# Optimization experiments

Hardware: AMD Instinct MI355X
Metric: run time of the kernel (lower is better)

The kernel has to match this reference:

```python
import jax, jax.numpy as jnp
import numpy as np

B, S, R, H = 32, 512, 49, 768


def setup_inputs() -> dict:
    key = jax.random.key(0)
    ks = jax.random.split(key, 32)
    rn = lambda i, shape, s=1.0: jax.random.normal(ks[i], shape, dtype=jnp.float32) * s
    W = 0.05  # weight init scale to keep tanh/softmax in a sane range
    return {
        'text_features': rn(0, (B, S, H)),
        'img_features': rn(1, (B, R, H)),
        't1_w': rn(2, (H, H), W), 't1_b': rn(3, (H,), W),
        'i1_w': rn(4, (H, H), W),
        'a1_w': rn(5, (2 * H,), W), 'a1_b': rn(6, (), W),
        't2_w': rn(7, (H, H), W),
        'i2_w': rn(8, (H, H), W), 'i2_b': rn(9, (H,), W),
        'a2_w': rn(10, (2 * H,), W), 'a2_b': rn(11, (), W),
        'gt_w': rn(12, (H, H), W), 'gt_b': rn(13, (H,), W),
        'gi_w': rn(14, (H, H), W), 'gi_b': rn(15, (H,), W),
        'gg_w': rn(16, (2 * H, 1), W), 'gg_b': rn(17, (1,), W),
        'ft_w': rn(18, (H, H), W),
        'fm_w': rn(19, (H, H), W), 'fm_b': rn(20, (H,), W),
        'fg_w': rn(21, (2 * H, 1), W), 'fg_b': rn(22, (1,), W),
        'fr_w': rn(23, (H, H), W), 'fr_b': rn(24, (H,), W),
    }


def reference(text_features, img_features, t1_w, t1_b, i1_w, a1_w, a1_b,
              t2_w, i2_w, i2_b, a2_w, a2_b, gt_w, gt_b, gi_w, gi_b,
              gg_w, gg_b, ft_w, fm_w, fm_b, fg_w, fg_b, fr_w, fr_b):
    H = text_features.shape[-1]
    # --- CoAttention, stage 1 (text attends over image regions) ---
    # tanh(concat) is elementwise and att_linear_1 is rank-1, so split the score:
    # score[b,s,r] = tanh(t1(x_s)) . a1[:H] + tanh(i1(y_r)) . a1[H:] + b
    t_sc = jnp.tanh(text_features @ t1_w + t1_b) @ a1_w[:H]          # (B,S)
    i_sc = jnp.tanh(img_features @ i1_w) @ a1_w[H:]                  # (B,R)
    visual_att = jax.nn.softmax(t_sc[:, :, None] + i_sc[:, None, :] + a1_b, axis=-1)  # (B,S,R)
    att_img = jnp.einsum('bsr,brh->bsh', visual_att, img_features)   # (B,S,H)
    # --- CoAttention, stage 2 (attended-image queries attend over text) ---
    # concat order is [img, text] -> a2[:H] pairs with img part
    q_sc = jnp.tanh(att_img @ i2_w + i2_b) @ a2_w[:H]                # (B,S)
    k_sc = jnp.tanh(text_features @ t2_w) @ a2_w[H:]                 # (B,S)
    textual_att = jax.nn.softmax(q_sc[:, :, None] + k_sc[:, None, :] + a2_b, axis=-1)  # (B,S,S)
    att_text = jnp.einsum('bij,bjh->bih', textual_att, text_features)  # (B,S,H)
    # --- GMF gated fusion ---
    new_img = jnp.tanh(att_img @ gi_w + gi_b)
    new_txt = jnp.tanh(att_text @ gt_w + gt_b)
    gate = jax.nn.sigmoid(jnp.concatenate([new_img, new_txt], axis=-1) @ gg_w + gg_b)  # (B,S,1)
    multimodal = gate * new_img + (1.0 - gate) * new_txt
    # --- filtration gate ---
    concat_feat = jnp.concatenate([text_features @ ft_w, multimodal @ fm_w + fm_b], axis=-1)
    fgate = jax.nn.sigmoid(concat_feat @ fg_w + fg_b)                # (B,S,1)
    return fgate * jnp.tanh(multimodal @ fr_w + fr_b)
```

## Files before the change

### kernel.cpp

```cpp
#include <hip/hip_runtime.h>
#include <hip/hip_bf16.h>
#include <math.h>

constexpr int BD = 32;
constexpr int SD = 512;
constexpr int RD = 49;
constexpr int HD = 768;
constexpr int MT = BD * SD;
constexpr int MI = BD * RD;
constexpr int NP = 12;
constexpr int MBT = MT / 128;
constexpr int MBI = 13;
constexpr int NWG = (MBT + MBI) * 6;
constexpr int NT2 = HD / 64;

typedef __bf16 bf16;
typedef __bf16 bf16x4 __attribute__((ext_vector_type(4)));
typedef __bf16 bf16x8 __attribute__((ext_vector_type(8)));
typedef float f32x4 __attribute__((ext_vector_type(4)));

#define GLOAD_LDS16(g, l) __builtin_amdgcn_global_load_lds( \
    (__attribute__((address_space(1))) void*)(g),           \
    (__attribute__((address_space(3))) void*)(l), 16, 0, 0)

__device__ __forceinline__ float fast_tanh(float x) {
    const float e = __expf(2.f * x);
    return 1.f - 2.f / (e + 1.f);
}

__global__ __launch_bounds__(256) void prep_text(
    const float* __restrict__ text, const float* __restrict__ v_f,
    bf16* __restrict__ text_bf, float* __restrict__ s_txt)
{
    const int row = blockIdx.x * 4 + (threadIdx.x >> 6);
    const int lane = threadIdx.x & 63;
    const float* tr = text + (size_t)row * HD;
    bf16* tb = text_bf + (size_t)row * HD;
    float acc = 0.f;
    #pragma unroll
    for (int c = 0; c < 3; ++c) {
        const int o = c * 256 + lane * 4;
        const f32x4 x = *(const f32x4*)(tr + o);
        const f32x4 v = *(const f32x4*)(v_f + o);
        bf16x4 b; b[0] = (bf16)x[0]; b[1] = (bf16)x[1]; b[2] = (bf16)x[2]; b[3] = (bf16)x[3];
        *(bf16x4*)(tb + o) = b;
        acc += x[0] * v[0] + x[1] * v[1] + x[2] * v[2] + x[3] * v[3];
    }
    for (int off = 32; off; off >>= 1) acc += __shfl_xor(acc, off);
    if (lane == 0) s_txt[row] = acc;
}

__global__ __launch_bounds__(256) void prep_misc(
    const float* __restrict__ ft_w, const float* __restrict__ fm_w,
    const float* __restrict__ fm_b, const float* __restrict__ fg_w,
    float* __restrict__ v_f, float* __restrict__ v_m, float* __restrict__ c_m,
    const float* __restrict__ img, bf16* __restrict__ img_bf,
    const float* __restrict__ t2_w, const float* __restrict__ i1_w,
    bf16* __restrict__ wt_t, bf16* __restrict__ wt_i)
{
    __shared__ float tile[64][65];
    const int bid = blockIdx.x;
    if (bid < 385) {
        const int idx = bid * 4 + (threadIdx.x >> 6);
        const int lane = threadIdx.x & 63;
        const float* row; const float* vecp; float* outp;
        if (idx < HD)            { row = ft_w + (size_t)idx * HD;        vecp = fg_w;      outp = v_f + idx; }
        else if (idx < 2 * HD)   { row = fm_w + (size_t)(idx - HD) * HD; vecp = fg_w + HD; outp = v_m + (idx - HD); }
        else if (idx == 2 * HD)  { row = fm_b;                           vecp = fg_w + HD; outp = c_m; }
        else return;
        float acc = 0.f;
        #pragma unroll
        for (int i = 0; i < HD / 64; ++i) acc += row[lane + 64 * i] * vecp[lane + 64 * i];
        for (int off = 32; off; off >>= 1) acc += __shfl_xor(acc, off);
        if (lane == 0) *outp = acc;
    } else if (bid < 385 + 588) {
        const int i = (bid - 385) * 256 + threadIdx.x;
        const int n8 = BD * RD * HD / 8;
        if (i >= n8) return;
        const size_t o = (size_t)i * 8;
        const f32x4 x0 = *(const f32x4*)(img + o);
        const f32x4 x1 = *(const f32x4*)(img + o + 4);
        bf16x8 b;
        b[0]=(bf16)x0[0]; b[1]=(bf16)x0[1]; b[2]=(bf16)x0[2]; b[3]=(bf16)x0[3];
        b[4]=(bf16)x1[0]; b[5]=(bf16)x1[1]; b[6]=(bf16)x1[2]; b[7]=(bf16)x1[3];
        *(bf16x8*)(img_bf + o) = b;
    } else {
        const int idx2 = bid - (385 + 588);
        const int z = idx2 / 144, rem = idx2 % 144;
        const int bx = rem % 12, by = rem / 12;
        const float* W = z ? i1_w : t2_w;
        bf16* Wt = z ? wt_i : wt_t;
        const int k0 = bx * 64, n0 = by * 64;
        const int t = threadIdx.x;
        const int rb = t >> 6, c = t & 63;
        #pragma unroll
        for (int i = 0; i < 16; ++i) {
            const int r = rb + i * 4;
            tile[r][c] = W[(size_t)(k0 + r) * HD + n0 + c];
        }
        __syncthreads();
        #pragma unroll
        for (int i = 0; i < 16; ++i) {
            const int r = rb + i * 4;
            Wt[(size_t)(n0 + r) * HD + k0 + c] = (bf16)tile[c][r];
        }
    }
}

__global__ __launch_bounds__(256, 4) void gemm2(
    const bf16* __restrict__ Atext, const bf16* __restrict__ WtT,
    const float* __restrict__ vecT, float* __restrict__ partT,
    const bf16* __restrict__ Aimg, const bf16* __restrict__ WtI,
    const float* __restrict__ vecI, float* __restrict__ partI)
{
    __shared__ __align__(16) bf16 As[16 * 512];
    __shared__ __align__(16) bf16 Bs[16 * 512];

    const int bid = blockIdx.x;
    const int q = NWG / 8, r = NWG % 8;
    const int xcd = bid % 8, sidx = bid / 8;
    const int o = (xcd < r ? xcd * (q + 1) : r * (q + 1) + (xcd - r) * q) + sidx;
    const int mb = o / 6, nb = o % 6;

    const bool isT = mb < MBT;
    const bf16* A    = isT ? Atext : Aimg;
    const bf16* Wt   = isT ? WtT : WtI;
    const float* vec = isT ? vecT : vecI;
    float* part      = isT ? partT : partI;
    const int m0 = (isT ? mb : mb - MBT) * 128;
    const int n0 = nb * 128;

    const int t = threadIdx.x;
    const int w = t >> 6, lane = t & 63;
    const int quad = lane >> 4, l16 = lane & 15;
    const int wm2 = (w >> 1) * 64, wn2 = (w & 1) * 64;

    const bf16* Ag = A  + (size_t)(m0 + l16) * HD + quad * 8;
    const bf16* Bg = Wt + (size_t)(n0 + l16) * HD + quad * 8;

    f32x4 acc[4][4] = {};

    for (int tt = 0; tt < NT2; ++tt) {
        const int kk = tt * 64;
        #pragma unroll
        for (int h = 0; h < 2; ++h) {
            #pragma unroll
            for (int j = 0; j < 2; ++j) {
                const int rc = 2 * w + j;
                GLOAD_LDS16(Ag + (size_t)rc * 16 * HD + kk + h * 32, As + (h * 8 + rc) * 512);
                GLOAD_LDS16(Bg + (size_t)rc * 16 * HD + kk + h * 32, Bs + (h * 8 + rc) * 512);
            }
        }
        __syncthreads();

        #pragma unroll
        for (int h = 0; h < 2; ++h) {
            bf16x8 af[4], bg4[4];
            #pragma unroll
            for (int f = 0; f < 4; ++f) {
                af[f]  = *(const bf16x8*)(As + (h * 8 + wm2 / 16 + f) * 512 + lane * 8);
                bg4[f] = *(const bf16x8*)(Bs + (h * 8 + wn2 / 16 + f) * 512 + lane * 8);
            }
            #pragma unroll
            for (int fi = 0; fi < 4; ++fi)
                #pragma unroll
                for (int fj = 0; fj < 4; ++fj)
                    acc[fi][fj] = __builtin_amdgcn_mfma_f32_16x16x32_bf16(af[fi], bg4[fj], acc[fi][fj], 0, 0, 0);
        }
        __syncthreads();
    }

    float vv[4];
    #pragma unroll
    for (int fj = 0; fj < 4; ++fj) vv[fj] = vec[n0 + wn2 + fj * 16 + l16];

    #pragma unroll
    for (int fi = 0; fi < 4; ++fi) {
        #pragma unroll
        for (int reg = 0; reg < 4; ++reg) {
            float p = 0.f;
            #pragma unroll
            for (int fj = 0; fj < 4; ++fj)
                p += fast_tanh(acc[fi][fj][reg]) * vv[fj];
            p += __shfl_xor(p, 1);
            p += __shfl_xor(p, 2);
            p += __shfl_xor(p, 4);
            p += __shfl_xor(p, 8);
            if (l16 == 0) {
                const int row = m0 + wm2 + fi * 16 + quad * 4 + reg;
                part[(size_t)row * NP + nb * 2 + (w & 1)] = p;
            }
        }
    }
}

__global__ __launch_bounds__(256) void red_soft(
    const float* __restrict__ k_part, const float* __restrict__ i_part,
    float* __restrict__ k_sc, float* __restrict__ i_sc)
{
    __shared__ float red[4];
    if (blockIdx.x < BD) {
        const int b = blockIdx.x, t = threadIdx.x;
        const float* p0 = k_part + ((size_t)b * SD + t) * NP;
        const float* p1 = k_part + ((size_t)b * SD + 256 + t) * NP;
        float x0 = 0.f, x1 = 0.f;
        #pragma unroll
        for (int j = 0; j < 3; ++j) {
            const f32x4 a = *(const f32x4*)(p0 + j * 4);
            const f32x4 c = *(const f32x4*)(p1 + j * 4);
            x0 += a[0] + a[1] + a[2] + a[3];
            x1 += c[0] + c[1] + c[2] + c[3];
        }
        float m = fmaxf(x0, x1);
        for (int off = 32; off; off >>= 1) m = fmaxf(m, __shfl_xor(m, off));
        if ((t & 63) == 0) red[t >> 6] = m;
        __syncthreads();
        m = fmaxf(fmaxf(red[0], red[1]), fmaxf(red[2], red[3]));
        const float e0 = expf(x0 - m), e1 = expf(x1 - m);
        float s = e0 + e1;
        for (int off = 32; off; off >>= 1) s += __shfl_xor(s, off);
        __syncthreads();
        if ((t & 63) == 0) red[t >> 6] = s;
        __syncthreads();
        s = red[0] + red[1] + red[2] + red[3];
        k_sc[b * SD + t] = e0 / s;
        k_sc[b * SD + 256 + t] = e1 / s;
    } else {
        const int b = blockIdx.x - BD, l = threadIdx.x;
        if (l < 64) {
            float x = -1e30f;
            if (l < RD) {
                const float* p = i_part + ((size_t)(b * RD + l)) * NP;
                float s0 = 0.f;
                #pragma unroll
                for (int j = 0; j < 3; ++j) {
                    const f32x4 a = *(const f32x4*)(p + j * 4);
                    s0 += a[0] + a[1] + a[2] + a[3];
                }
                x = s0;
            }
            float m = x;
            for (int off = 32; off; off >>= 1) m = fmaxf(m, __shfl_xor(m, off));
            float e = (l < RD) ? expf(x - m) : 0.f;
            float s = e;
            for (int off = 32; off; off >>= 1) s += __shfl_xor(s, off);
            if (l < RD) i_sc[b * RD + l] = e / s;
        }
    }
}

__global__ __launch_bounds__(256) void wsum_both(
    const float* __restrict__ P1, const float* __restrict__ img,
    float* __restrict__ aimg,
    const float* __restrict__ P2, const bf16* __restrict__ text_bf,
    float* __restrict__ ws_part)
{
    __shared__ float Ps[SD];
    const int bid = blockIdx.x;
    if (bid < 96) {
        const int b = bid & 31, hy = bid >> 5;
        const int h = hy * 256 + threadIdx.x;
        for (int j = threadIdx.x; j < RD; j += 256) Ps[j] = P1[b * RD + j];
        __syncthreads();
        float acc = 0.f;
        const float* Xb = img + (size_t)b * RD * HD + h;
        for (int j = 0; j < RD; ++j) acc += Ps[j] * Xb[(size_t)j * HD];
        aimg[b * HD + h] = acc;
    } else {
        const int idx = bid - 96;
        const int q = idx / 96, rem = idx % 96;
        const int b = rem & 31, hy = rem >> 5;
        const int h = hy * 256 + threadIdx.x;
        if (threadIdx.x < 128) Ps[threadIdx.x] = P2[b * SD + q * 128 + threadIdx.x];
        __syncthreads();
        float acc = 0.f;
        const bf16* Xb = text_bf + (size_t)b * SD * HD + (size_t)(q * 128) * HD + h;
        #pragma unroll 8
        for (int j = 0; j < 128; ++j) acc += Ps[j] * (float)Xb[(size_t)j * HD];
        ws_part[((size_t)(b * 4 + q)) * HD + h] = acc;
    }
}

__global__ __launch_bounds__(256) void ni_nt_kernel(
    const float* __restrict__ aimg, const float* __restrict__ ws_part,
    const float* __restrict__ gi_w, const float* __restrict__ gi_b,
    const float* __restrict__ gt_w, const float* __restrict__ gt_b,
    float* __restrict__ ni, float* __restrict__ nt)
{
    const int b = blockIdx.x, n0 = blockIdx.y * 64, which = blockIdx.z;
    const float* W = which ? gt_w : gi_w;
    const float* bias = which ? gt_b : gi_b;
    float* Y = which ? nt : ni;

    __shared__ float Xs[HD];
    __shared__ float partial[4][64];
    const int t = threadIdx.x;
    if (which) {
        for (int h = t; h < HD; h += 256)
            Xs[h] = ws_part[((size_t)(b * 4 + 0)) * HD + h] + ws_part[((size_t)(b * 4 + 1)) * HD + h]
                  + ws_part[((size_t)(b * 4 + 2)) * HD + h] + ws_part[((size_t)(b * 4 + 3)) * HD + h];
    } else {
        for (int h = t; h < HD; h += 256) Xs[h] = aimg[b * HD + h];
    }
    __syncthreads();
    const int n = n0 + (t & 63), kq = t >> 6;
    float acc = 0.f;
    const float* Wp = W + (size_t)(kq * 192) * HD + n;
    #pragma unroll 8
    for (int h = 0; h < 192; ++h) acc += Xs[kq * 192 + h] * Wp[(size_t)h * HD];
    partial[kq][t & 63] = acc;
    __syncthreads();
    if (t < 64) {
        const float s = partial[0][t] + partial[1][t] + partial[2][t] + partial[3][t];
        Y[b * HD + n0 + t] = tanhf(s + bias[n0 + t]);
    }
}

__global__ __launch_bounds__(256) void gateT(
    const float* __restrict__ ni, const float* __restrict__ nt,
    const float* __restrict__ gg_w, const float* __restrict__ gg_b,
    const float* __restrict__ v_m, const float* __restrict__ c_m,
    const float* __restrict__ fg_b,
    const float* __restrict__ fr_w, const float* __restrict__ fr_b,
    float* __restrict__ T, float* __restrict__ s_mm)
{
    const int b = blockIdx.x, n0 = blockIdx.y * 64, t = threadIdx.x;
    __shared__ float Ni[HD], Nt[HD], Mm[HD];
    __shared__ float partial[4][64];
    __shared__ float red[4];
    __shared__ float gsh;

    float acc = 0.f;
    for (int n = t; n < HD; n += 256) {
        const float vi = ni[b * HD + n], vt = nt[b * HD + n];
        Ni[n] = vi; Nt[n] = vt;
        acc += vi * gg_w[n] + vt * gg_w[HD + n];
    }
    for (int off = 32; off; off >>= 1) acc += __shfl_xor(acc, off);
    if ((t & 63) == 0) red[t >> 6] = acc;
    __syncthreads();
    if (t == 0) gsh = 1.f / (1.f + expf(-(red[0] + red[1] + red[2] + red[3] + gg_b[0])));
    __syncthreads();
    const float g = gsh;
    float a2 = 0.f;
    for (int n = t; n < HD; n += 256) {
        const float m = g * Ni[n] + (1.f - g) * Nt[n];
        Mm[n] = m;
        a2 += m * v_m[n];
    }
    __syncthreads();
    const int n = n0 + (t & 63), kq = t >> 6;
    float tacc = 0.f;
    const float* Wp = fr_w + (size_t)(kq * 192) * HD + n;
    #pragma unroll 8
    for (int h = 0; h < 192; ++h) tacc += Mm[kq * 192 + h] * Wp[(size_t)h * HD];
    partial[kq][t & 63] = tacc;
    if (blockIdx.y == 0) {
        for (int off = 32; off; off >>= 1) a2 += __shfl_xor(a2, off);
        __syncthreads();
        if ((t & 63) == 0) red[t >> 6] = a2;
        __syncthreads();
        if (t == 0) s_mm[b] = red[0] + red[1] + red[2] + red[3] + *c_m + fg_b[0];
    } else {
        __syncthreads();
    }
    __syncthreads();
    if (t < 64) {
        const float s = partial[0][t] + partial[1][t] + partial[2][t] + partial[3][t];
        T[b * HD + n0 + t] = tanhf(s + fr_b[n0 + t]);
    }
}

__global__ __launch_bounds__(256) void out_kernel(const float* __restrict__ s_txt,
                                                  const float* __restrict__ s_mm,
                                                  const float* __restrict__ T,
                                                  float* __restrict__ out) {
    const size_t idx = ((size_t)blockIdx.x * 256 + threadIdx.x) * 4;
    const int h = (int)(idx % HD);
    const int bs = (int)(idx / HD);
    const int b = bs >> 9;
    float f = s_txt[bs] + s_mm[b];
    f = 1.f / (1.f + expf(-f));
    const float* Tp = T + b * HD + h;
    f32x4 o;
    o[0] = f * Tp[0]; o[1] = f * Tp[1]; o[2] = f * Tp[2]; o[3] = f * Tp[3];
    *(f32x4*)(out + idx) = o;
}

extern "C" void kernel_launch(void* const* d_in, const int* in_sizes, int n_in,
                              void* d_out, int out_size, void* d_ws, size_t ws_size,
                              hipStream_t stream) {
    const float* text = (const float*)d_in[0];
    const float* img  = (const float*)d_in[1];
    const float* i1_w = (const float*)d_in[4];
    const float* a1_w = (const float*)d_in[5];
    const float* t2_w = (const float*)d_in[7];
    const float* a2_w = (const float*)d_in[10];
    const float* gt_w = (const float*)d_in[12];
    const float* gt_b = (const float*)d_in[13];
    const float* gi_w = (const float*)d_in[14];
    const float* gi_b = (const float*)d_in[15];
    const float* gg_w = (const float*)d_in[16];
    const float* gg_b = (const float*)d_in[17];
    const float* ft_w = (const float*)d_in[18];
    const float* fm_w = (const float*)d_in[19];
    const float* fm_b = (const float*)d_in[20];
    const float* fg_w = (const float*)d_in[21];
    const float* fg_b = (const float*)d_in[22];
    const float* fr_w = (const float*)d_in[23];
    const float* fr_b = (const float*)d_in[24];
    float* out = (float*)d_out;

    float* sc_ = out;
    float* i_part  = sc_;
    float* k_part  = sc_ + 38400;
    float* i_sc    = sc_ + 431616;
    float* k_sc    = sc_ + 433216;
    float* aimg    = sc_ + 449600;
    float* v_f     = sc_ + 498752;
    float* v_m     = sc_ + 499520;
    float* c_m     = sc_ + 500288;
    float* ws_part = sc_ + 500352;
    float* ni      = sc_ + 598656;
    float* nt      = sc_ + 623232;
    bf16* text_bf  = (bf16*)(sc_ + 672384);
    bf16* img_bf   = (bf16*)(sc_ + 6963840);
    bf16* wt_t     = (bf16*)(sc_ + 7565952);
    bf16* wt_i     = (bf16*)(sc_ + 7860864);

    float* ws    = (float*)d_ws;
    float* s_txt = ws;
    float* s_mm  = ws + 16384;
    float* T     = ws + 16448;

    prep_misc<<<dim3(385 + 588 + 288), dim3(256), 0, stream>>>(
        ft_w, fm_w, fm_b, fg_w, v_f, v_m, c_m, img, img_bf, t2_w, i1_w, wt_t, wt_i);
    prep_text<<<dim3(MT / 4), dim3(256), 0, stream>>>(text, v_f, text_bf, s_txt);
    gemm2<<<dim3(NWG), dim3(256), 0, stream>>>(
        text_bf, wt_t, a2_w + HD, k_part, img_bf, wt_i, a1_w + HD, i_part);
    red_soft<<<dim3(2 * BD), dim3(256), 0, stream>>>(k_part, i_part, k_sc, i_sc);
    wsum_both<<<dim3(96 + 384), dim3(256), 0, stream>>>(
        i_sc, img, aimg, k_sc, text_bf, ws_part);
    ni_nt_kernel<<<dim3(BD, HD / 64, 2), dim3(256), 0, stream>>>(
        aimg, ws_part, gi_w, gi_b, gt_w, gt_b, ni, nt);
    gateT<<<dim3(BD, HD / 64), dim3(256), 0, stream>>>(
        ni, nt, gg_w, gg_b, v_m, c_m, fg_b, fr_w, fr_b, T, s_mm);
    out_kernel<<<dim3((MT * HD / 4) / 256), dim3(256), 0, stream>>>(s_txt, s_mm, T, out);
}
```

Measured before the change: 266.5 us.

## Fuse softmax into weighted sums and batch tail GEMVs across the batch

Merges the score-reduction and softmax kernel into the weighted-sum kernel, so each block recomputes its batch softmax and normalises at the end instead of writing probabilities and text partial sums to global memory. The text weighted sum now spans all 512 rows per block instead of four partial blocks, which cuts parallelism (192 blocks instead of 480) but removes one launch and the partial reduction. The gi/gt and fr GEMVs are restructured so each block handles all 32 batch rows for 64 output columns and reuses each weight load across 4 rows per wave. That cuts redundant weight reads, but the GEMV grids shrink to 24 and 12 blocks, leaving most CUs idle.

```diff
diff --git a/kernel.cpp b/kernel.cpp
--- a/kernel.cpp
+++ b/kernel.cpp
@@ -194,129 +194,120 @@
     }
 }
 
-__global__ __launch_bounds__(256) void red_soft(
+__global__ __launch_bounds__(256) void wsum2(
     const float* __restrict__ k_part, const float* __restrict__ i_part,
-    float* __restrict__ k_sc, float* __restrict__ i_sc)
-{
+    const bf16* __restrict__ text_bf, const float* __restrict__ img,
+    float* __restrict__ atxt, float* __restrict__ aimg)
+{
+    __shared__ float S[SD];
     __shared__ float red[4];
-    if (blockIdx.x < BD) {
-        const int b = blockIdx.x, t = threadIdx.x;
-        const float* p0 = k_part + ((size_t)b * SD + t) * NP;
-        const float* p1 = k_part + ((size_t)b * SD + 256 + t) * NP;
-        float x0 = 0.f, x1 = 0.f;
-        #pragma unroll
-        for (int j = 0; j < 3; ++j) {
-            const f32x4 a = *(const f32x4*)(p0 + j * 4);
-            const f32x4 c = *(const f32x4*)(p1 + j * 4);
-            x0 += a[0] + a[1] + a[2] + a[3];
-            x1 += c[0] + c[1] + c[2] + c[3];
-        }
-        float m = fmaxf(x0, x1);
+    const int bid = blockIdx.x;
+    const bool isText = bid < 96;
+    const int idx = isText ? bid : bid - 96;
+    const int b = idx & 31, hy = idx >> 5;
+    const int t = threadIdx.x;
+
+    if (isText) {
+        for (int j = t; j < SD; j += 256) {
+            const float* p = k_part + (size_t)(b * SD + j) * NP;
+            float s = 0.f;
+            #pragma unroll
+            for (int u = 0; u < 3; ++u) {
+                const f32x4 a = *(const f32x4*)(p + u * 4);
+                s += a[0] + a[1] + a[2] + a[3];
+            }
+            S[j] = s;
+        }
+        __syncthreads();
+        float m = fmaxf(S[t], S[t + 256]);
         for (int off = 32; off; off >>= 1) m = fmaxf(m, __shfl_xor(m, off));
         if ((t & 63) == 0) red[t >> 6] = m;
         __syncthreads();
         m = fmaxf(fmaxf(red[0], red[1]), fmaxf(red[2], red[3]));
-        const float e0 = expf(x0 - m), e1 = expf(x1 - m);
-        float s = e0 + e1;
-        for (int off = 32; off; off >>= 1) s += __shfl_xor(s, off);
-        __syncthreads();
-        if ((t & 63) == 0) red[t >> 6] = s;
-        __syncthreads();
-        s = red[0] + red[1] + red[2] + red[3];
-        k_sc[b * SD + t] = e0 / s;
-        k_sc[b * SD + 256 + t] = e1 / s;
+        float lsum = 0.f;
+        {
+            const float e0 = __expf(S[t] - m), e1 = __expf(S[t + 256] - m);
+            S[t] = e0; S[t + 256] = e1;
+            lsum = e0 + e1;
+        }
+        for (int off = 32; off; off >>= 1) lsum += __shfl_xor(lsum, off);
+        __syncthreads();
+        if ((t & 63) == 0) red[t >> 6] = lsum;
+        __syncthreads();
+        const float inv = 1.f / (red[0] + red[1] + red[2] + red[3]);
+        const int h = hy * 256 + t;
+        const bf16* Xb = text_bf + (size_t)b * SD * HD + h;
+        float acc = 0.f;
+        #pragma unroll 8
+        for (int j = 0; j < SD; ++j) acc += S[j] * (float)Xb[(size_t)j * HD];
+        atxt[b * HD + h] = acc * inv;
     } else {
-        const int b = blockIdx.x - BD, l = threadIdx.x;
-        if (l < 64) {
-            float x = -1e30f;
-            if (l < RD) {
-                const float* p = i_part + ((size_t)(b * RD + l)) * NP;
-                float s0 = 0.f;
+        if (t < 64) {
+            float s0 = -1e30f;
+            if (t < RD) {
+                const float* p = i_part + (size_t)(b * RD + t) * NP;
+                float s = 0.f;
                 #pragma unroll
-                for (int j = 0; j < 3; ++j) {
-                    const f32x4 a = *(const f32x4*)(p + j * 4);
-                    s0 += a[0] + a[1] + a[2] + a[3];
+                for (int u = 0; u < 3; ++u) {
+                    const f32x4 a = *(const f32x4*)(p + u * 4);
+                    s += a[0] + a[1] + a[2] + a[3];
                 }
-                x = s0;
+                s0 = s;
             }
-            float m = x;
+            float m = s0;
             for (int off = 32; off; off >>= 1) m = fmaxf(m, __shfl_xor(m, off));
-            float e = (l < RD) ? expf(x - m) : 0.f;
-            float s = e;
-            for (int off = 32; off; off >>= 1) s += __shfl_xor(s, off);
-            if (l < RD) i_sc[b * RD + l] = e / s;
-        }
-    }
-}
-
-__global__ __launch_bounds__(256) void wsum_both(
-    const float* __restrict__ P1, const float* __restrict__ img,
-    float* __restrict__ aimg,
-    const float* __restrict__ P2, const bf16* __restrict__ text_bf,
-    float* __restrict__ ws_part)
-{
-    __shared__ float Ps[SD];
-    const int bid = blockIdx.x;
-    if (bid < 96) {
-        const int b = bid & 31, hy = bid >> 5;
-        const int h = hy * 256 + threadIdx.x;
-        for (int j = threadIdx.x; j < RD; j += 256) Ps[j] = P1[b * RD + j];
-        __syncthreads();
+            float e = (t < RD) ? __expf(s0 - m) : 0.f;
+            float lsum = e;
+            for (int off = 32; off; off >>= 1) lsum += __shfl_xor(lsum, off);
+            if (t < RD) S[t] = e;
+            if (t == 0) red[0] = 1.f / lsum;
+        }
+        __syncthreads();
+        const float inv = red[0];
+        const int h = hy * 256 + t;
+        const float* Xb = img + (size_t)b * RD * HD + h;
         float acc = 0.f;
-        const float* Xb = img + (size_t)b * RD * HD + h;
-        for (int j = 0; j < RD; ++j) acc += Ps[j] * Xb[(size_t)j * HD];
-        aimg[b * HD + h] = acc;
-    } else {
-        const int idx = bid - 96;
-        const int q = idx / 96, rem = idx % 96;
-        const int b = rem & 31, hy = rem >> 5;
-        const int h = hy * 256 + threadIdx.x;
-        if (threadIdx.x < 128) Ps[threadIdx.x] = P2[b * SD + q * 128 + threadIdx.x];
-        __syncthreads();
-        float acc = 0.f;
-        const bf16* Xb = text_bf + (size_t)b * SD * HD + (size_t)(q * 128) * HD + h;
-        #pragma unroll 8
-        for (int j = 0; j < 128; ++j) acc += Ps[j] * (float)Xb[(size_t)j * HD];
-        ws_part[((size_t)(b * 4 + q)) * HD + h] = acc;
-    }
-}
-
-__global__ __launch_bounds__(256) void ni_nt_kernel(
-    const float* __restrict__ aimg, const float* __restrict__ ws_part,
+        #pragma unroll 7
+        for (int j = 0; j < RD; ++j) acc += S[j] * Xb[(size_t)j * HD];
+        aimg[b * HD + h] = acc * inv;
+    }
+}
+
+__global__ __launch_bounds__(512) void ni_nt2(
+    const float* __restrict__ aimg, const float* __restrict__ atxt,
     const float* __restrict__ gi_w, const float* __restrict__ gi_b,
     const float* __restrict__ gt_w, const float* __restrict__ gt_b,
     float* __restrict__ ni, float* __restrict__ nt)
 {
-    const int b = blockIdx.x, n0 = blockIdx.y * 64, which = blockIdx.z;
+    const int which = blockIdx.y;
+    const float* X = which ? atxt : aimg;
     const float* W = which ? gt_w : gi_w;
     const float* bias = which ? gt_b : gi_b;
     float* Y = which ? nt : ni;
 
-    __shared__ float Xs[HD];
-    __shared__ float partial[4][64];
     const int t = threadIdx.x;
-    if (which) {
-        for (int h = t; h < HD; h += 256)
-            Xs[h] = ws_part[((size_t)(b * 4 + 0)) * HD + h] + ws_part[((size_t)(b * 4 + 1)) * HD + h]
-                  + ws_part[((size_t)(b * 4 + 2)) * HD + h] + ws_part[((size_t)(b * 4 + 3)) * HD + h];
-    } else {
-        for (int h = t; h < HD; h += 256) Xs[h] = aimg[b * HD + h];
-    }
-    __syncthreads();
-    const int n = n0 + (t & 63), kq = t >> 6;
-    float acc = 0.f;
-    const float* Wp = W + (size_t)(kq * 192) * HD + n;
-    #pragma unroll 8
-    for (int h = 0; h < 192; ++h) acc += Xs[kq * 192 + h] * Wp[(size_t)h * HD];
-    partial[kq][t & 63] = acc;
-    __syncthreads();
-    if (t < 64) {
-        const float s = partial[0][t] + partial[1][t] + partial[2][t] + partial[3][t];
-        Y[b * HD + n0 + t] = tanhf(s + bias[n0 + t]);
-    }
-}
-
-__global__ __launch_bounds__(256) void gateT(
+    const int c = t & 63;
+    const int wv = __builtin_amdgcn_readfirstlane(t >> 6);
+    const int n = blockIdx.x * 64 + c;
+    const float* Xb = X + (size_t)(4 * wv) * HD;
+
+    float a0 = 0.f, a1 = 0.f, a2 = 0.f, a3 = 0.f;
+    #pragma unroll 4
+    for (int k = 0; k < HD; ++k) {
+        const float w0 = W[(size_t)k * HD + n];
+        a0 += Xb[k] * w0;
+        a1 += Xb[HD + k] * w0;
+        a2 += Xb[2 * HD + k] * w0;
+        a3 += Xb[3 * HD + k] * w0;
+    }
+    const float bb = bias[n];
+    Y[(size_t)(4 * wv + 0) * HD + n] = tanhf(a0 + bb);
+    Y[(size_t)(4 * wv + 1) * HD + n] = tanhf(a1 + bb);
+    Y[(size_t)(4 * wv + 2) * HD + n] = tanhf(a2 + bb);
+    Y[(size_t)(4 * wv + 3) * HD + n] = tanhf(a3 + bb);
+}
+
+__global__ __launch_bounds__(512) void gateT2(
     const float* __restrict__ ni, const float* __restrict__ nt,
     const float* __restrict__ gg_w, const float* __restrict__ gg_b,
     const float* __restrict__ v_m, const float* __restrict__ c_m,
@@ -324,51 +315,65 @@
     const float* __restrict__ fr_w, const float* __restrict__ fr_b,
     float* __restrict__ T, float* __restrict__ s_mm)
 {
-    const int b = blockIdx.x, n0 = blockIdx.y * 64, t = threadIdx.x;
-    __shared__ float Ni[HD], Nt[HD], Mm[HD];
-    __shared__ float partial[4][64];
-    __shared__ float red[4];
-    __shared__ float gsh;
-
-    float acc = 0.f;
-    for (int n = t; n < HD; n += 256) {
-        const float vi = ni[b * HD + n], vt = nt[b * HD + n];
-        Ni[n] = vi; Nt[n] = vt;
-        acc += vi * gg_w[n] + vt * gg_w[HD + n];
-    }
-    for (int off = 32; off; off >>= 1) acc += __shfl_xor(acc, off);
-    if ((t & 63) == 0) red[t >> 6] = acc;
+    __shared__ float Mm[HD][36];
+    __shared__ float g_sh[BD];
+    __shared__ float sm_sh[BD];
+    const int t = threadIdx.x;
+
+    {
+        const int b = t >> 4, l = t & 15;
+        const float* nib = ni + (size_t)b * HD;
+        const float* ntb = nt + (size_t)b * HD;
+        float dgi = 0.f, dgt = 0.f, dvi = 0.f, dvt = 0.f;
+        for (int j = l; j < HD; j += 16) {
+            const float a = nib[j], d = ntb[j];
+            dgi += a * gg_w[j];
+            dgt += d * gg_w[HD + j];
+            dvi += a * v_m[j];
+            dvt += d * v_m[j];
+        }
+        #pragma unroll
+        for (int off = 8; off; off >>= 1) {
+            dgi += __shfl_xor(dgi, off);
+            dgt += __shfl_xor(dgt, off);
+            dvi += __shfl_xor(dvi, off);
+            dvt += __shfl_xor(dvt, off);
+        }
+        if (l == 0) {
+            const float g = 1.f / (1.f + expf(-(dgi + dgt + gg_b[0])));
+            g_sh[b] = g;
+            sm_sh[b] = g * dvi + (1.f - g) * dvt;
+        }
+    }
     __syncthreads();
-    if (t == 0) gsh = 1.f / (1.f + expf(-(red[0] + red[1] + red[2] + red[3] + gg_b[0])));
+    if (blockIdx.x == 0 && t < BD) s_mm[t] = sm_sh[t] + c_m[0] + fg_b[0];
+
+    for (int b = 0; b < BD; ++b) {
+        const float g = g_sh[b];
+        const float* nib = ni + (size_t)b * HD;
+        const float* ntb = nt + (size_t)b * HD;
+        for (int h = t; h < HD; h += 512)
+            Mm[h][b] = g * nib[h] + (1.f - g) * ntb[h];
+    }
     __syncthreads();
-    const float g = gsh;
-    float a2 = 0.f;
-    for (int n = t; n < HD; n += 256) {
-        const float m = g * Ni[n] + (1.f - g) * Nt[n];
-        Mm[n] = m;
-        a2 += m * v_m[n];
-    }
-    __syncthreads();
-    const int n = n0 + (t & 63), kq = t >> 6;
-    float tacc = 0.f;
-    const float* Wp = fr_w + (size_t)(kq * 192) * HD + n;
-    #pragma unroll 8
-    for (int h = 0; h < 192; ++h) tacc += Mm[kq * 192 + h] * Wp[(size_t)h * HD];
-    partial[kq][t & 63] = tacc;
-    if (blockIdx.y == 0) {
-        for (int off = 32; off; off >>= 1) a2 += __shfl_xor(a2, off);
-        __syncthreads();
-        if ((t & 63) == 0) red[t >> 6] = a2;
-        __syncthreads();
-        if (t == 0) s_mm[b] = red[0] + red[1] + red[2] + red[3] + *c_m + fg_b[0];
-    } else {
-        __syncthreads();
-    }
-    __syncthreads();
-    if (t < 64) {
-        const float s = partial[0][t] + partial[1][t] + partial[2][t] + partial[3][t];
-        T[b * HD + n0 + t] = tanhf(s + fr_b[n0 + t]);
-    }
+
+    const int c = t & 63;
+    const int wv = __builtin_amdgcn_readfirstlane(t >> 6);
+    const int n = blockIdx.x * 64 + c;
+    f32x4 acc = {0.f, 0.f, 0.f, 0.f};
+    #pragma unroll 4
+    for (int k = 0; k < HD; ++k) {
+        const float w0 = fr_w[(size_t)k * HD + n];
+        const f32x4 mv = *(const f32x4*)&Mm[k][4 * wv];
+        acc[0] += mv[0] * w0;
+        acc[1] += mv[1] * w0;
+        acc[2] += mv[2] * w0;
+        acc[3] += mv[3] * w0;
+    }
+    const float bb = fr_b[n];
+    #pragma unroll
+    for (int j = 0; j < 4; ++j)
+        T[(size_t)(4 * wv + j) * HD + n] = tanhf(acc[j] + bb);
 }
 
 __global__ __launch_bounds__(256) void out_kernel(const float* __restrict__ s_txt,
@@ -414,13 +419,11 @@
     float* sc_ = out;
     float* i_part  = sc_;
     float* k_part  = sc_ + 38400;
-    float* i_sc    = sc_ + 431616;
-    float* k_sc    = sc_ + 433216;
     float* aimg    = sc_ + 449600;
+    float* atxt    = sc_ + 474176;
     float* v_f     = sc_ + 498752;
     float* v_m     = sc_ + 499520;
     float* c_m     = sc_ + 500288;
-    float* ws_part = sc_ + 500352;
     float* ni      = sc_ + 598656;
     float* nt      = sc_ + 623232;
     bf16* text_bf  = (bf16*)(sc_ + 672384);
@@ -438,12 +441,11 @@
     prep_text<<<dim3(MT / 4), dim3(256), 0, stream>>>(text, v_f, text_bf, s_txt);
     gemm2<<<dim3(NWG), dim3(256), 0, stream>>>(
         text_bf, wt_t, a2_w + HD, k_part, img_bf, wt_i, a1_w + HD, i_part);
-    red_soft<<<dim3(2 * BD), dim3(256), 0, stream>>>(k_part, i_part, k_sc, i_sc);
-    wsum_both<<<dim3(96 + 384), dim3(256), 0, stream>>>(
-        i_sc, img, aimg, k_sc, text_bf, ws_part);
-    ni_nt_kernel<<<dim3(BD, HD / 64, 2), dim3(256), 0, stream>>>(
-        aimg, ws_part, gi_w, gi_b, gt_w, gt_b, ni, nt);
-    gateT<<<dim3(BD, HD / 64), dim3(256), 0, stream>>>(
+    wsum2<<<dim3(192), dim3(256), 0, stream>>>(
+        k_part, i_part, text_bf, img, atxt, aimg);
+    ni_nt2<<<dim3(12, 2), dim3(512), 0, stream>>>(
+        aimg, atxt, gi_w, gi_b, gt_w, gt_b, ni, nt);
+    gateT2<<<dim3(12), dim3(512), 0, stream>>>(
         ni, nt, gg_w, gg_b, v_m, c_m, fg_b, fr_w, fr_b, T, s_mm);
     out_kernel<<<dim3((MT * HD / 4) / 256), dim3(256), 0, stream>>>(s_txt, s_mm, T, out);
 }
```

After: 471.4 us. 76.9% more time.

## Double-buffer larger 256x256 score GEMM and fuse softmax into weighted-sum kernel

Applied to the files above, without the earlier changes.

The score GEMM goes from 128x128 tiles with 256 threads to 256x256 tiles with 512 threads. It double-buffers LDS and uses explicit vmcnt waits so the next K-slab loads while the current one computes. The separate softmax kernel is folded into the weighted-sum kernel, which removes a launch and the k_sc/i_sc round trip. The text weighted sum is no longer split four ways along the sequence, so each block now loops over all 512 rows, with fewer blocks. The larger tiles yield far fewer workgroups (about 198) and higher register pressure, which may underfill the GPU.

```diff
diff --git a/kernel.cpp b/kernel.cpp
--- a/kernel.cpp
+++ b/kernel.cpp
@@ -8,11 +8,12 @@
 constexpr int HD = 768;
 constexpr int MT = BD * SD;
 constexpr int MI = BD * RD;
-constexpr int NP = 12;
-constexpr int MBT = MT / 128;
-constexpr int MBI = 13;
-constexpr int NWG = (MBT + MBI) * 6;
-constexpr int NT2 = HD / 64;
+constexpr int NP = 6;
+constexpr int MBT3 = MT / 256;
+constexpr int MBI3 = 7;
+constexpr int NB3 = 3;
+constexpr int NWG3 = (MBT3 + MBI3) * NB3;
+constexpr int NT3 = HD / 64;
 
 typedef __bf16 bf16;
 typedef __bf16 bf16x4 __attribute__((ext_vector_type(4)));
@@ -22,6 +23,9 @@
 #define GLOAD_LDS16(g, l) __builtin_amdgcn_global_load_lds( \
     (__attribute__((address_space(1))) void*)(g),           \
     (__attribute__((address_space(3))) void*)(l), 16, 0, 0)
+#define BAR() __builtin_amdgcn_s_barrier()
+#define SCHED_FENCE() __builtin_amdgcn_sched_barrier(0)
+#define WAITV(n) asm volatile("s_waitcnt vmcnt(" #n ")" ::: "memory")
 
 __device__ __forceinline__ float fast_tanh(float x) {
     const float e = __expf(2.f * x);
@@ -107,72 +111,97 @@
     }
 }
 
-__global__ __launch_bounds__(256, 4) void gemm2(
+__global__ __launch_bounds__(512, 2) void gemm3(
     const bf16* __restrict__ Atext, const bf16* __restrict__ WtT,
     const float* __restrict__ vecT, float* __restrict__ partT,
     const bf16* __restrict__ Aimg, const bf16* __restrict__ WtI,
     const float* __restrict__ vecI, float* __restrict__ partI)
 {
-    __shared__ __align__(16) bf16 As[16 * 512];
-    __shared__ __align__(16) bf16 Bs[16 * 512];
+    __shared__ __align__(16) bf16 As[2 * 16384];
+    __shared__ __align__(16) bf16 Bs[2 * 16384];
 
     const int bid = blockIdx.x;
-    const int q = NWG / 8, r = NWG % 8;
+    const int q = NWG3 / 8, r = NWG3 % 8;
     const int xcd = bid % 8, sidx = bid / 8;
     const int o = (xcd < r ? xcd * (q + 1) : r * (q + 1) + (xcd - r) * q) + sidx;
-    const int mb = o / 6, nb = o % 6;
-
-    const bool isT = mb < MBT;
+    const int mb = o / NB3, nb = o % NB3;
+
+    const bool isT = mb < MBT3;
     const bf16* A    = isT ? Atext : Aimg;
     const bf16* Wt   = isT ? WtT : WtI;
     const float* vec = isT ? vecT : vecI;
     float* part      = isT ? partT : partI;
-    const int m0 = (isT ? mb : mb - MBT) * 128;
-    const int n0 = nb * 128;
+    const int m0 = (isT ? mb : mb - MBT3) * 256;
+    const int n0 = nb * 256;
 
     const int t = threadIdx.x;
     const int w = t >> 6, lane = t & 63;
     const int quad = lane >> 4, l16 = lane & 15;
-    const int wm2 = (w >> 1) * 64, wn2 = (w & 1) * 64;
+    const int wm_idx = w & 3, wn_idx = w >> 2;
+    const int wm2 = wm_idx * 64, wn2 = wn_idx * 128;
 
     const bf16* Ag = A  + (size_t)(m0 + l16) * HD + quad * 8;
     const bf16* Bg = Wt + (size_t)(n0 + l16) * HD + quad * 8;
 
-    f32x4 acc[4][4] = {};
-
-    for (int tt = 0; tt < NT2; ++tt) {
-        const int kk = tt * 64;
-        #pragma unroll
-        for (int h = 0; h < 2; ++h) {
-            #pragma unroll
-            for (int j = 0; j < 2; ++j) {
-                const int rc = 2 * w + j;
-                GLOAD_LDS16(Ag + (size_t)rc * 16 * HD + kk + h * 32, As + (h * 8 + rc) * 512);
-                GLOAD_LDS16(Bg + (size_t)rc * 16 * HD + kk + h * 32, Bs + (h * 8 + rc) * 512);
-            }
-        }
-        __syncthreads();
-
-        #pragma unroll
-        for (int h = 0; h < 2; ++h) {
-            bf16x8 af[4], bg4[4];
-            #pragma unroll
-            for (int f = 0; f < 4; ++f) {
-                af[f]  = *(const bf16x8*)(As + (h * 8 + wm2 / 16 + f) * 512 + lane * 8);
-                bg4[f] = *(const bf16x8*)(Bs + (h * 8 + wn2 / 16 + f) * 512 + lane * 8);
-            }
-            #pragma unroll
-            for (int fi = 0; fi < 4; ++fi)
-                #pragma unroll
-                for (int fj = 0; fj < 4; ++fj)
-                    acc[fi][fj] = __builtin_amdgcn_mfma_f32_16x16x32_bf16(af[fi], bg4[fj], acc[fi][fj], 0, 0, 0);
-        }
-        __syncthreads();
-    }
-
-    float vv[4];
+    f32x4 acc[4][8] = {};
+
+#define STAGE3(tt, bb) {                                                     \
+    const int kk = (tt) * 64;                                                \
+    _Pragma("unroll")                                                        \
+    for (int h = 0; h < 2; ++h) {                                            \
+        _Pragma("unroll")                                                    \
+        for (int j = 0; j < 2; ++j) {                                        \
+            const int rc = 2 * w + j;                                        \
+            GLOAD_LDS16(Ag + (size_t)rc * 16 * HD + kk + h * 32,             \
+                        As + (bb) * 16384 + (h * 16 + rc) * 512);            \
+            GLOAD_LDS16(Bg + (size_t)rc * 16 * HD + kk + h * 32,             \
+                        Bs + (bb) * 16384 + (h * 16 + rc) * 512);            \
+        }                                                                    \
+    }                                                                        \
+}
+
+#define COMPUTE3(bb) {                                                       \
+    _Pragma("unroll")                                                        \
+    for (int h = 0; h < 2; ++h) {                                            \
+        bf16x8 af[4], bg[8];                                                 \
+        _Pragma("unroll")                                                    \
+        for (int fi = 0; fi < 4; ++fi)                                       \
+            af[fi] = *(const bf16x8*)(As + (bb) * 16384 +                    \
+                       (h * 16 + wm_idx * 4 + fi) * 512 + lane * 8);         \
+        _Pragma("unroll")                                                    \
+        for (int fj = 0; fj < 8; ++fj)                                       \
+            bg[fj] = *(const bf16x8*)(Bs + (bb) * 16384 +                    \
+                       (h * 16 + wn_idx * 8 + fj) * 512 + lane * 8);         \
+        _Pragma("unroll")                                                    \
+        for (int fi = 0; fi < 4; ++fi)                                       \
+            _Pragma("unroll")                                                \
+            for (int fj = 0; fj < 8; ++fj)                                   \
+                acc[fi][fj] = __builtin_amdgcn_mfma_f32_16x16x32_bf16(       \
+                    af[fi], bg[fj], acc[fi][fj], 0, 0, 0);                   \
+    }                                                                        \
+}
+
+    STAGE3(0, 0);
+    for (int tt = 0; tt < NT3 - 1; ++tt) {
+        STAGE3(tt + 1, (tt + 1) & 1);
+        WAITV(8);
+        BAR();
+        SCHED_FENCE();
+        COMPUTE3(tt & 1);
+        SCHED_FENCE();
+        BAR();
+    }
+    WAITV(0);
+    BAR();
+    SCHED_FENCE();
+    COMPUTE3((NT3 - 1) & 1);
+
+#undef STAGE3
+#undef COMPUTE3
+
+    float vv[8];
     #pragma unroll
-    for (int fj = 0; fj < 4; ++fj) vv[fj] = vec[n0 + wn2 + fj * 16 + l16];
+    for (int fj = 0; fj < 8; ++fj) vv[fj] = vec[n0 + wn2 + fj * 16 + l16];
 
     #pragma unroll
     for (int fi = 0; fi < 4; ++fi) {
@@ -180,7 +209,7 @@
         for (int reg = 0; reg < 4; ++reg) {
             float p = 0.f;
             #pragma unroll
-            for (int fj = 0; fj < 4; ++fj)
+            for (int fj = 0; fj < 8; ++fj)
                 p += fast_tanh(acc[fi][fj][reg]) * vv[fj];
             p += __shfl_xor(p, 1);
             p += __shfl_xor(p, 2);
@@ -188,106 +217,93 @@
             p += __shfl_xor(p, 8);
             if (l16 == 0) {
                 const int row = m0 + wm2 + fi * 16 + quad * 4 + reg;
-                part[(size_t)row * NP + nb * 2 + (w & 1)] = p;
+                part[(size_t)row * NP + nb * 2 + wn_idx] = p;
             }
         }
     }
 }
 
-__global__ __launch_bounds__(256) void red_soft(
+__global__ __launch_bounds__(256) void wsum2(
     const float* __restrict__ k_part, const float* __restrict__ i_part,
-    float* __restrict__ k_sc, float* __restrict__ i_sc)
-{
+    const bf16* __restrict__ text_bf, const float* __restrict__ img,
+    float* __restrict__ atxt, float* __restrict__ aimg)
+{
+    __shared__ float S[SD];
     __shared__ float red[4];
-    if (blockIdx.x < BD) {
-        const int b = blockIdx.x, t = threadIdx.x;
-        const float* p0 = k_part + ((size_t)b * SD + t) * NP;
-        const float* p1 = k_part + ((size_t)b * SD + 256 + t) * NP;
-        float x0 = 0.f, x1 = 0.f;
-        #pragma unroll
-        for (int j = 0; j < 3; ++j) {
-            const f32x4 a = *(const f32x4*)(p0 + j * 4);
-            const f32x4 c = *(const f32x4*)(p1 + j * 4);
-            x0 += a[0] + a[1] + a[2] + a[3];
-            x1 += c[0] + c[1] + c[2] + c[3];
-        }
-        float m = fmaxf(x0, x1);
+    const int bid = blockIdx.x;
+    const bool isText = bid < 96;
+    const int idx = isText ? bid : bid - 96;
+    const int b = idx & 31, hy = idx >> 5;
+    const int t = threadIdx.x;
+
+    if (isText) {
+        for (int j = t; j < SD; j += 256) {
+            const float* p = k_part + (size_t)(b * SD + j) * NP;
+            float s = 0.f;
+            #pragma unroll
+            for (int u = 0; u < NP; ++u) s += p[u];
+            S[j] = s;
+        }
+        __syncthreads();
+        float m = fmaxf(S[t], S[t + 256]);
         for (int off = 32; off; off >>= 1) m = fmaxf(m, __shfl_xor(m, off));
         if ((t & 63) == 0) red[t >> 6] = m;
         __syncthreads();
         m = fmaxf(fmaxf(red[0], red[1]), fmaxf(red[2], red[3]));
-        const float e0 = expf(x0 - m), e1 = expf(x1 - m);
-        float s = e0 + e1;
-        for (int off = 32; off; off >>= 1) s += __shfl_xor(s, off);
-        __syncthreads();
-        if ((t & 63) == 0) red[t >> 6] = s;
-        __syncthreads();
-        s = red[0] + red[1] + red[2] + red[3];
-        k_sc[b * SD + t] = e0 / s;
-        k_sc[b * SD + 256 + t] = e1 / s;
+        float lsum = 0.f;
+        {
+            const float e0 = __expf(S[t] - m), e1 = __expf(S[t + 256] - m);
+            S[t] = e0; S[t + 256] = e1;
+            lsum = e0 + e1;
+        }
+        for (int off = 32; off; off >>= 1) lsum += __shfl_xor(lsum, off);
+        __syncthreads();
+        if ((t & 63) == 0) red[t >> 6] = lsum;
+        __syncthreads();
+        const float inv = 1.f / (red[0] + red[1] + red[2] + red[3]);
+        const int h = hy * 256 + t;
+        const bf16* Xb = text_bf + (size_t)b * SD * HD + h;
+        float acc = 0.f;
+        #pragma unroll 8
+        for (int j = 0; j < SD; ++j) acc += S[j] * (float)Xb[(size_t)j * HD];
+        atxt[b * HD + h] = acc * inv;
     } else {
-        const int b = blockIdx.x - BD, l = threadIdx.x;
-        if (l < 64) {
-            float x = -1e30f;
-            if (l < RD) {
-                const float* p = i_part + ((size_t)(b * RD + l)) * NP;
-                float s0 = 0.f;
+        if (t < 64) {
+            float s0 = -1e30f;
+            if (t < RD) {
+                const float* p = i_part + (size_t)(b * RD + t) * NP;
+                float s = 0.f;
                 #pragma unroll
-                for (int j = 0; j < 3; ++j) {
-                    const f32x4 a = *(const f32x4*)(p + j * 4);
-                    s0 += a[0] + a[1] + a[2] + a[3];
-                }
-                x = s0;
+                for (int u = 0; u < NP; ++u) s += p[u];
+                s0 = s;
             }
-            float m = x;
+            float m = s0;
             for (int off = 32; off; off >>= 1) m = fmaxf(m, __shfl_xor(m, off));
-            float e = (l < RD) ? expf(x - m) : 0.f;
-            float s = e;
-            for (int off = 32; off; off >>= 1) s += __shfl_xor(s, off);
-            if (l < RD) i_sc[b * RD + l] = e / s;
-        }
-    }
-}
-
-__global__ __launch_bounds__(256) void wsum_both(
-    const float* __restrict__ P1, const float* __restrict__ img,
-    float* __restrict__ aimg,
-    const float* __restrict__ P2, const bf16* __restrict__ text_bf,
-    float* __restrict__ ws_part)
-{
-    __shared__ float Ps[SD];
-    const int bid = blockIdx.x;
-    if (bid < 96) {
-        const int b = bid & 31, hy = bid >> 5;
-        const int h = hy * 256 + threadIdx.x;
-        for (int j = threadIdx.x; j < RD; j += 256) Ps[j] = P1[b * RD + j];
-        __syncthreads();
+            float e = (t < RD) ? __expf(s0 - m) : 0.f;
+            float lsum = e;
+            for (int off = 32; off; off >>= 1) lsum += __shfl_xor(lsum, off);
+            if (t < RD) S[t] = e;
+            if (t == 0) red[0] = 1.f / lsum;
+        }
+        __syncthreads();
+        const float inv = red[0];
+        const int h = hy * 256 + t;
+        const float* Xb = img + (size_t)b * RD * HD + h;
         float acc = 0.f;
-        const float* Xb = img + (size_t)b * RD * HD + h;
-        for (int j = 0; j < RD; ++j) acc += Ps[j] * Xb[(size_t)j * HD];
-        aimg[b * HD + h] = acc;
-    } else {
-        const int idx = bid - 96;
-        const int q = idx / 96, rem = idx % 96;
-        const int b = rem & 31, hy = rem >> 5;
-        const int h = hy * 256 + threadIdx.x;
-        if (threadIdx.x < 128) Ps[threadIdx.x] = P2[b * SD + q * 128 + threadIdx.x];
-        __syncthreads();
-        float acc = 0.f;
-        const bf16* Xb = text_bf + (size_t)b * SD * HD + (size_t)(q * 128) * HD + h;
-        #pragma unroll 8
-        for (int j = 0; j < 128; ++j) acc += Ps[j] * (float)Xb[(size_t)j * HD];
-        ws_part[((size_t)(b * 4 + q)) * HD + h] = acc;
+        #pragma unroll 7
+        for (int j = 0; j < RD; ++j) acc += S[j] * Xb[(size_t)j * HD];
+        aimg[b * HD + h] = acc * inv;
     }
 }
 
 __global__ __launch_bounds__(256) void ni_nt_kernel(
-    const float* __restrict__ aimg, const float* __restrict__ ws_part,
+    const float* __restrict__ aimg, const float* __restrict__ atxt,
     const float* __restrict__ gi_w, const float* __restrict__ gi_b,
     const float* __restrict__ gt_w, const float* __restrict__ gt_b,
     float* __restrict__ ni, float* __restrict__ nt)
 {
     const int b = blockIdx.x, n0 = blockIdx.y * 64, which = blockIdx.z;
+    const float* X = which ? atxt : aimg;
     const float* W = which ? gt_w : gi_w;
     const float* bias = which ? gt_b : gi_b;
     float* Y = which ? nt : ni;
@@ -295,13 +311,7 @@
     __shared__ float Xs[HD];
     __shared__ float partial[4][64];
     const int t = threadIdx.x;
-    if (which) {
-        for (int h = t; h < HD; h += 256)
-            Xs[h] = ws_part[((size_t)(b * 4 + 0)) * HD + h] + ws_part[((size_t)(b * 4 + 1)) * HD + h]
-                  + ws_part[((size_t)(b * 4 + 2)) * HD + h] + ws_part[((size_t)(b * 4 + 3)) * HD + h];
-    } else {
-        for (int h = t; h < HD; h += 256) Xs[h] = aimg[b * HD + h];
-    }
+    for (int h = t; h < HD; h += 256) Xs[h] = X[b * HD + h];
     __syncthreads();
     const int n = n0 + (t & 63), kq = t >> 6;
     float acc = 0.f;
@@ -414,13 +424,11 @@
     float* sc_ = out;
     float* i_part  = sc_;
     float* k_part  = sc_ + 38400;
-    float* i_sc    = sc_ + 431616;
-    float* k_sc    = sc_ + 433216;
     float* aimg    = sc_ + 449600;
+    float* atxt    = sc_ + 474176;
     float* v_f     = sc_ + 498752;
     float* v_m     = sc_ + 499520;
     float* c_m     = sc_ + 500288;
-    float* ws_part = sc_ + 500352;
     float* ni      = sc_ + 598656;
     float* nt      = sc_ + 623232;
     bf16* text_bf  = (bf16*)(sc_ + 672384);
@@ -436,13 +444,12 @@
     prep_misc<<<dim3(385 + 588 + 288), dim3(256), 0, stream>>>(
         ft_w, fm_w, fm_b, fg_w, v_f, v_m, c_m, img, img_bf, t2_w, i1_w, wt_t, wt_i);
     prep_text<<<dim3(MT / 4), dim3(256), 0, stream>>>(text, v_f, text_bf, s_txt);
-    gemm2<<<dim3(NWG), dim3(256), 0, stream>>>(
+    gemm3<<<dim3(NWG3), dim3(512), 0, stream>>>(
         text_bf, wt_t, a2_w + HD, k_part, img_bf, wt_i, a1_w + HD, i_part);
-    red_soft<<<dim3(2 * BD), dim3(256), 0, stream>>>(k_part, i_part, k_sc, i_sc);
-    wsum_both<<<dim3(96 + 384), dim3(256), 0, stream>>>(
-        i_sc, img, aimg, k_sc, text_bf, ws_part);
+    wsum2<<<dim3(192), dim3(256), 0, stream>>>(
+        k_part, i_part, text_bf, img, atxt, aimg);
     ni_nt_kernel<<<dim3(BD, HD / 64, 2), dim3(256), 0, stream>>>(
-        aimg, ws_part, gi_w, gi_b, gt_w, gt_b, ni, nt);
+        aimg, atxt, gi_w, gi_b, gt_w, gt_b, ni, nt);
     gateT<<<dim3(BD, HD / 64), dim3(256), 0, stream>>>(
         ni, nt, gg_w, gg_b, v_m, c_m, fg_b, fr_w, fr_b, T, s_mm);
     out_kernel<<<dim3((MT * HD / 4) / 256), dim3(256), 0, stream>>>(s_txt, s_mm, T, out);
```

Result: slower. 271.8 us (+2.0%).
